# Kernel tuning notes

Hardware: AMD Instinct MI355X
Metric: run time of the kernel (lower is better)

Reference implementation:

```python
import jax, jax.numpy as jnp
import numpy as np
from jax import lax

N_Q = 4          # kernel_size**2 for Q_conv(kernel_size=2)
DIM = 16         # 2**N_Q statevector dimension
N_LAYERS = 3

# --- static circuit constants -------------------------------------------

def _cnot_np(c, t):
    # PennyLane convention: wire 0 is the most-significant bit.
    M = np.zeros((DIM, DIM), np.complex64)
    for s in range(DIM):
        s2 = s ^ (1 << (N_Q - 1 - t)) if (s >> (N_Q - 1 - c)) & 1 else s
        M[s2, s] = 1.0
    return jnp.asarray(M)

# StronglyEntanglingLayers: layer l uses range r = l % (n_wires-1) + 1
_CNOTS = {r: [_cnot_np(i, (i + r) % N_Q) for i in range(N_Q)] for r in (1, 2, 3)}

_ZDIAG = jnp.asarray(np.array(
    [[1.0 - 2.0 * ((s >> (N_Q - 1 - w)) & 1) for w in range(N_Q)] for s in range(DIM)],
    np.float32))  # (16, 4): diag of PauliZ on each wire


def _rot(p):
    # qml.Rot(phi, theta, omega) = RZ(omega) RY(theta) RZ(phi)
    phi, th, om = p[0], p[1], p[2]
    c, s = jnp.cos(th / 2), jnp.sin(th / 2)
    r0 = jnp.stack([jnp.exp(-1j * (phi + om) / 2) * c, -jnp.exp(1j * (phi - om) / 2) * s])
    r1 = jnp.stack([jnp.exp(-1j * (phi - om) / 2) * s, jnp.exp(1j * (phi + om) / 2) * c])
    return jnp.stack([r0, r1]).astype(jnp.complex64)


def _circuit_unitary(qw):
    # qw: (3, 4, 3). One StronglyEntanglingLayers block of 3 layers,
    # which the qnode applies n_layers=3 times with the SAME weights.
    U = jnp.eye(DIM, dtype=jnp.complex64)
    for l in range(N_LAYERS):
        L = _rot(qw[l, 0])
        for q in range(1, N_Q):
            L = jnp.kron(L, _rot(qw[l, q]))
        for C in _CNOTS[l + 1]:
            L = C @ L
        U = L @ U
    return U @ U @ U


def _quanv(x, qw):
    # x: (B, 1, 44, 44); k = stride = 2 -> non-overlapping 2x2 patches.
    B, H = x.shape[0], x.shape[-1]
    o = H // 2  # 22
    patches = x.reshape(B, o, 2, o, 2).transpose(0, 1, 3, 2, 4).reshape(-1, 4)
    # AngleEmbedding (RX) on |0000> gives a product state.
    a = jnp.cos(patches / 2).astype(jnp.complex64)
    b = (-1j * jnp.sin(patches / 2)).astype(jnp.complex64)
    w = jnp.stack([a, b], axis=-1)  # (N, 4, 2)
    psi0 = jnp.einsum('na,nb,nc,nd->nabcd', w[:, 0], w[:, 1], w[:, 2], w[:, 3]).reshape(-1, DIM)
    psi = psi0 @ _circuit_unitary(qw).T  # (N, 16)
    probs = psi.real ** 2 + psi.imag ** 2
    e = probs @ _ZDIAG  # (N, 4) expvals of PauliZ per wire
    return e.reshape(B, o * o, N_Q).transpose(0, 2, 1).reshape(B, N_Q, o, o).astype(x.dtype)


def _conv(x, w, b, stride):
    y = lax.conv_general_dilated(x, w, (stride, stride), 'VALID',
                                 dimension_numbers=('NCHW', 'OIHW', 'NCHW'))
    return y + b[None, :, None, None]


def _maxpool(x, k, s):
    return lax.reduce_window(x, -jnp.inf, lax.max, (1, 1, k, k), (1, 1, s, s), 'VALID')


def setup_inputs() -> dict:
    key = jax.random.key(0)
    ks = jax.random.split(key, 18)
    B = 256
    f32 = jnp.float32
    return {
        'x': jax.random.normal(ks[0], (B, 1, 186, 186), f32),
        'conv1_w': jax.random.normal(ks[1], (1, 1, 8, 8), f32) * 0.1,
        'conv1_b': jax.random.normal(ks[2], (1,), f32) * 0.05,
        'q_w': jax.random.uniform(ks[3], (3, 4, 3), f32, 0.0, 2.0 * np.pi),
        'conv2_w': jax.random.normal(ks[4], (32, 4, 4, 4), f32) * 0.1,
        'conv2_b': jax.random.normal(ks[5], (32,), f32) * 0.05,
        'conv3_w': jax.random.normal(ks[6], (64, 32, 4, 4), f32) * 0.05,
        'conv3_b': jax.random.normal(ks[7], (64,), f32) * 0.05,
        'conv4_w': jax.random.normal(ks[8], (128, 64, 4, 4), f32) * 0.03,
        'conv4_b': jax.random.normal(ks[9], (128,), f32) * 0.05,
        'fc1_w': jax.random.normal(ks[10], (128, 3200), f32) * 0.02,
        'fc1_b': jax.random.normal(ks[11], (128,), f32) * 0.05,
        'fc2_w': jax.random.normal(ks[12], (64, 128), f32) * 0.09,
        'fc2_b': jax.random.normal(ks[13], (64,), f32) * 0.05,
        'fc3_w': jax.random.normal(ks[14], (16, 64), f32) * 0.12,
        'fc3_b': jax.random.normal(ks[15], (16,), f32) * 0.05,
        'fc4_w': jax.random.normal(ks[16], (2, 16), f32) * 0.25,
        'fc4_b': jax.random.normal(ks[17], (2,), f32) * 0.05,
    }


def reference(x, conv1_w, conv1_b, q_w, conv2_w, conv2_b, conv3_w, conv3_b,
              conv4_w, conv4_b, fc1_w, fc1_b, fc2_w, fc2_b, fc3_w, fc3_b,
              fc4_w, fc4_b):
    h = _maxpool(jnp.tanh(_conv(x, conv1_w, conv1_b, 2)), 4, 2) * (np.pi / 2)
    h = jax.nn.relu(_quanv(h, q_w))                       # (B, 4, 22, 22)
    h = _maxpool(jax.nn.relu(_conv(h, conv2_w, conv2_b, 1)), 4, 1)
    h = _maxpool(jax.nn.relu(_conv(h, conv3_w, conv3_b, 1)), 2, 1)
    h = jax.nn.relu(_conv(h, conv4_w, conv4_b, 2))        # (B, 128, 5, 5)
    h = h.reshape(h.shape[0], -1)
    h = jax.nn.relu(h @ fc1_w.T + fc1_b)   # dropout: eval mode = identity
    h = jax.nn.relu(h @ fc2_w.T + fc2_b)
    h = jax.nn.relu(h @ fc3_w.T + fc3_b)
    return jax.nn.log_softmax(h @ fc4_w.T + fc4_b, axis=1)
```

## Files before the change

kernel.cpp:

```cpp
#include <hip/hip_runtime.h>
#include <hip/hip_bf16.h>
#include <math.h>


__device__ __forceinline__ float2 cmul(float2 a, float2 b) {
    return make_float2(a.x * b.x - a.y * b.y, a.x * b.y + a.y * b.x);
}
__device__ __forceinline__ float2 cfma(float2 a, float2 b, float2 acc) {
    acc.x += a.x * b.x - a.y * b.y;
    acc.y += a.x * b.y + a.y * b.x;
    return acc;
}

__global__ __launch_bounds__(256) void k_build_V(const float* __restrict__ qw,
                                                 float2* __restrict__ Vout) {
    __shared__ float2 rot[3][4][2][2];
    __shared__ float2 L[16][16];
    __shared__ float2 U[16][16];
    __shared__ float2 T[16][16];

    int tid = threadIdx.x;
    if (tid < 12) {
        int l = tid >> 2, q = tid & 3;
        float phi = qw[(l * 4 + q) * 3 + 0];
        float th  = qw[(l * 4 + q) * 3 + 1];
        float om  = qw[(l * 4 + q) * 3 + 2];
        float c, s;
        sincosf(0.5f * th, &s, &c);
        float sa, ca, sb, cb;
        sincosf(0.5f * (phi + om), &sa, &ca);
        sincosf(0.5f * (phi - om), &sb, &cb);
        rot[l][q][0][0] = make_float2( ca * c, -sa * c);
        rot[l][q][0][1] = make_float2(-cb * s, -sb * s);
        rot[l][q][1][0] = make_float2( cb * s, -sb * s);
        rot[l][q][1][1] = make_float2( ca * c,  sa * c);
    }
    int s = tid >> 4, t = tid & 15;
    U[s][t] = make_float2((s == t) ? 1.f : 0.f, 0.f);
    __syncthreads();

    for (int l = 0; l < 3; ++l) {
        int r = l + 1;
        int ss = s;
        for (int i = 3; i >= 0; --i) {
            int c_ = i, t_ = (i + r) & 3;
            if ((ss >> (3 - c_)) & 1) ss ^= 1 << (3 - t_);
        }
        float2 v = make_float2(1.f, 0.f);
        #pragma unroll
        for (int q = 0; q < 4; ++q) {
            int bs = (ss >> (3 - q)) & 1;
            int bt = (t  >> (3 - q)) & 1;
            v = cmul(v, rot[l][q][bs][bt]);
        }
        L[s][t] = v;
        __syncthreads();
        float2 acc = make_float2(0.f, 0.f);
        #pragma unroll
        for (int k = 0; k < 16; ++k) acc = cfma(L[s][k], U[k][t], acc);
        T[s][t] = acc;
        __syncthreads();
        U[s][t] = T[s][t];
        __syncthreads();
    }
    float2 acc = make_float2(0.f, 0.f);
    #pragma unroll
    for (int k = 0; k < 16; ++k) acc = cfma(U[s][k], U[k][t], acc);
    T[s][t] = acc;
    __syncthreads();
    acc = make_float2(0.f, 0.f);
    #pragma unroll
    for (int k = 0; k < 16; ++k) acc = cfma(T[s][k], U[k][t], acc);
    int pc = __popc(t) & 3;
    float2 v;
    if      (pc == 0) v = acc;
    else if (pc == 1) v = make_float2( acc.y, -acc.x);
    else if (pc == 2) v = make_float2(-acc.x, -acc.y);
    else              v = make_float2(-acc.y,  acc.x);
    Vout[s * 16 + t] = v;
}

__global__ __launch_bounds__(256) void k_wtrans(const float* __restrict__ w3,
                                                const float* __restrict__ w4,
                                                float* __restrict__ wt3,
                                                float* __restrict__ wt4) {
    int idx = blockIdx.x * 256 + threadIdx.x;
    if (idx < 32768) {
        int oc = idx & 63, tap = (idx >> 6) & 15, ic = idx >> 10;
        wt3[idx] = w3[oc * 512 + ic * 16 + tap];
    } else {
        int o = idx - 32768;
        int oc = o & 127, tap = (o >> 7) & 15, ic = o >> 11;
        wt4[o] = w4[oc * 1024 + ic * 16 + tap];
    }
}

__global__ __launch_bounds__(256) void k_conv1d(const float* __restrict__ x,
                                                const float* __restrict__ w,
                                                const float* __restrict__ bias,
                                                float* __restrict__ y) {
    int idx = blockIdx.x * 256 + threadIdx.x;
    int j = idx % 90;
    int t = idx / 90;
    int i = t % 90;
    int b = t / 90;
    const float* xb = x + b * 34596 + (2 * i) * 186 + 2 * j;
    float acc = bias[0];
    #pragma unroll
    for (int u = 0; u < 8; ++u) {
        const float* rp = xb + u * 186;
        float2 p0 = *(const float2*)(rp + 0);
        float2 p1 = *(const float2*)(rp + 2);
        float2 p2 = *(const float2*)(rp + 4);
        float2 p3 = *(const float2*)(rp + 6);
        acc = fmaf(w[u * 8 + 0], p0.x, acc);
        acc = fmaf(w[u * 8 + 1], p0.y, acc);
        acc = fmaf(w[u * 8 + 2], p1.x, acc);
        acc = fmaf(w[u * 8 + 3], p1.y, acc);
        acc = fmaf(w[u * 8 + 4], p2.x, acc);
        acc = fmaf(w[u * 8 + 5], p2.y, acc);
        acc = fmaf(w[u * 8 + 6], p3.x, acc);
        acc = fmaf(w[u * 8 + 7], p3.y, acc);
    }
    y[idx] = tanhf(acc);
}

__global__ __launch_bounds__(256) void k_pool1(const float* __restrict__ y,
                                               float* __restrict__ p) {
    int idx = blockIdx.x * 256 + threadIdx.x;
    int j = idx % 44;
    int t = idx / 44;
    int i = t % 44;
    int b = t / 44;
    const float* yb = y + b * 8100 + (2 * i) * 90 + 2 * j;
    float m = -INFINITY;
    #pragma unroll
    for (int u = 0; u < 4; ++u)
        #pragma unroll
        for (int v = 0; v < 4; ++v)
            m = fmaxf(m, yb[u * 90 + v]);
    p[idx] = m * 1.57079632679489662f;
}

__global__ __launch_bounds__(256) void k_quanv(const float* __restrict__ p,
                                               const float2* __restrict__ Vg,
                                               float* __restrict__ o) {
    __shared__ float2 V[256];
    V[threadIdx.x] = Vg[threadIdx.x];
    __syncthreads();

    int idx = blockIdx.x * 256 + threadIdx.x;
    int j = idx % 22;
    int t = idx / 22;
    int i = t % 22;
    int b = t / 22;
    const float* pb = p + b * 1936 + (2 * i) * 44 + 2 * j;
    float a0 = pb[0], a1 = pb[1], a2 = pb[44], a3 = pb[45];

    float cs[4], sn[4];
    sincosf(0.5f * a0, &sn[0], &cs[0]);
    sincosf(0.5f * a1, &sn[1], &cs[1]);
    sincosf(0.5f * a2, &sn[2], &cs[2]);
    sincosf(0.5f * a3, &sn[3], &cs[3]);

    float c[16];
    #pragma unroll
    for (int tt = 0; tt < 16; ++tt) {
        c[tt] = ((tt & 8) ? sn[0] : cs[0]) * ((tt & 4) ? sn[1] : cs[1]) *
                ((tt & 2) ? sn[2] : cs[2]) * ((tt & 1) ? sn[3] : cs[3]);
    }

    float e0 = 0.f, e1 = 0.f, e2 = 0.f, e3 = 0.f;
    #pragma unroll
    for (int s = 0; s < 16; ++s) {
        float re = 0.f, im = 0.f;
        #pragma unroll
        for (int tt = 0; tt < 16; ++tt) {
            float2 v = V[s * 16 + tt];
            re = fmaf(v.x, c[tt], re);
            im = fmaf(v.y, c[tt], im);
        }
        float pr = re * re + im * im;
        e0 += (s & 8) ? -pr : pr;
        e1 += (s & 4) ? -pr : pr;
        e2 += (s & 2) ? -pr : pr;
        e3 += (s & 1) ? -pr : pr;
    }
    float* ob = o + b * (4 * 484) + i * 22 + j;
    ob[0]    = fmaxf(e0, 0.f);
    ob[484]  = fmaxf(e1, 0.f);
    ob[968]  = fmaxf(e2, 0.f);
    ob[1452] = fmaxf(e3, 0.f);
}

__global__ __launch_bounds__(640) void k_conv2t(const float* __restrict__ x,
                                                const float* __restrict__ w,
                                                const float* __restrict__ bias,
                                                float* __restrict__ y) {
    __shared__ float Xs[4 * 22 * 28];
    __shared__ float Ws[32 * 68];
    int b = blockIdx.x;
    int tid = threadIdx.x;

    const float* xb = x + b * 1936;
    for (int k = tid; k < 1936; k += 640) {
        int ic = k / 484, rem = k % 484;
        int r = rem / 22, c = rem % 22;
        Xs[ic * 616 + r * 28 + c] = xb[k];
    }
    for (int k = tid; k < 2048; k += 640) {
        Ws[(k >> 6) * 68 + (k & 63)] = w[k];
    }
    __syncthreads();

    if (tid < 608) {
        int oc = tid / 19, i = tid % 19;
        float acc[19];
        float bv = bias[oc];
        #pragma unroll
        for (int j = 0; j < 19; ++j) acc[j] = bv;
        const float* wr = &Ws[oc * 68];
        #pragma unroll
        for (int ic = 0; ic < 4; ++ic) {
            #pragma unroll
            for (int u = 0; u < 4; ++u) {
                const float* rp = &Xs[ic * 616 + (i + u) * 28];
                float xr[22];
                #pragma unroll
                for (int k = 0; k < 5; ++k)
                    *(float4*)&xr[4 * k] = *(const float4*)(rp + 4 * k);
                *(float2*)&xr[20] = *(const float2*)(rp + 20);
                float4 wv = *(const float4*)(wr + ic * 16 + u * 4);
                #pragma unroll
                for (int j = 0; j < 19; ++j) {
                    acc[j] = fmaf(wv.x, xr[j],     acc[j]);
                    acc[j] = fmaf(wv.y, xr[j + 1], acc[j]);
                    acc[j] = fmaf(wv.z, xr[j + 2], acc[j]);
                    acc[j] = fmaf(wv.w, xr[j + 3], acc[j]);
                }
            }
        }
        float* yp = y + b * 11552 + oc * 361 + i * 19;
        #pragma unroll
        for (int j = 0; j < 19; ++j) yp[j] = fmaxf(acc[j], 0.f);
    }
}

__global__ __launch_bounds__(256) void k_pool2(const float* __restrict__ x,
                                               float* __restrict__ y) {
    int idx = blockIdx.x * 256 + threadIdx.x;
    int j = idx % 16;
    int t = idx / 16;
    int i = t % 16;
    int c = t / 16;
    const float* xb = x + c * 361 + i * 19 + j;
    float m = -INFINITY;
    #pragma unroll
    for (int u = 0; u < 4; ++u)
        #pragma unroll
        for (int v = 0; v < 4; ++v)
            m = fmaxf(m, xb[u * 19 + v]);
    y[idx] = m;
}

__global__ __launch_bounds__(448) void k_conv3x(const float* __restrict__ x,
                                                const float* __restrict__ wt3,
                                                const float* __restrict__ bias,
                                                float* __restrict__ y) {
    __shared__ float Xs[32 * 200];
    __shared__ float Rs[224 * 26];
    int bid = blockIdx.x;
    int b = bid >> 1, h = bid & 1;
    int r0 = h * 7;
    int nr = 7 - h;
    int tid = threadIdx.x;

    const float* xb = x + b * 8192 + r0 * 16;
    #pragma unroll
    for (int it = 0; it < 3; ++it) {
        int k = it * 448 + tid;
        if (k < 1280) {
            int ic = k / 40, rem = k % 40;
            int r = rem >> 2, c4 = rem & 3;
            if (r0 + r < 16) {
                float4 v = *(const float4*)(xb + ic * 256 + r * 16 + c4 * 4);
                *(float4*)(&Xs[ic * 200 + r * 20 + c4 * 4]) = v;
            }
        }
    }
    __syncthreads();

    int kg = (tid >= 224) ? 1 : 0;
    int t2 = tid - kg * 224;
    int ocp = t2 & 31, il = t2 >> 5;
    int oc0 = ocp * 2;

    float acc0[13], acc1[13];
    #pragma unroll
    for (int j = 0; j < 13; ++j) { acc0[j] = 0.f; acc1[j] = 0.f; }

    const float* wb = wt3 + kg * 16384 + oc0;
    for (int k = 0; k < 16; ++k) {
        const float* wp = wb + k * 1024;
        float2 cw[16];
        #pragma unroll
        for (int t = 0; t < 16; ++t) cw[t] = *(const float2*)(wp + t * 64);

        const float* xc = &Xs[(kg * 16 + k) * 200 + il * 20];
        #pragma unroll
        for (int u = 0; u < 4; ++u) {
            float xr[16];
            const float* rp = xc + u * 20;
            #pragma unroll
            for (int kk = 0; kk < 4; ++kk)
                *(float4*)&xr[4 * kk] = *(const float4*)(rp + 4 * kk);
            #pragma unroll
            for (int j = 0; j < 13; ++j) {
                #pragma unroll
                for (int v = 0; v < 4; ++v) {
                    acc0[j] = fmaf(cw[u * 4 + v].x, xr[j + v], acc0[j]);
                    acc1[j] = fmaf(cw[u * 4 + v].y, xr[j + v], acc1[j]);
                }
            }
        }
    }

    if (kg == 1) {
        float* rp = &Rs[t2 * 26];
        #pragma unroll
        for (int j = 0; j < 13; ++j) { rp[j] = acc0[j]; rp[13 + j] = acc1[j]; }
    }
    __syncthreads();

    if (kg == 0 && il < nr) {
        const float* rp = &Rs[t2 * 26];
        float bv0 = bias[oc0], bv1 = bias[oc0 + 1];
        float* yp = y + b * 10816 + oc0 * 169 + (r0 + il) * 13;
        #pragma unroll
        for (int j = 0; j < 13; ++j) {
            yp[j]       = fmaxf(acc0[j] + rp[j]      + bv0, 0.f);
            yp[169 + j] = fmaxf(acc1[j] + rp[13 + j] + bv1, 0.f);
        }
    }
}

__global__ __launch_bounds__(256) void k_pool3(const float* __restrict__ x,
                                               float* __restrict__ y) {
    int idx = blockIdx.x * 256 + threadIdx.x;
    int j = idx % 12;
    int t = idx / 12;
    int i = t % 12;
    int c = t / 12;
    const float* xb = x + c * 169 + i * 13 + j;
    float m = fmaxf(fmaxf(xb[0], xb[1]), fmaxf(xb[13], xb[14]));
    y[idx] = m;
}

__global__ __launch_bounds__(640) void k_conv4s(const float* __restrict__ x,
                                                const float* __restrict__ wt4,
                                                float* __restrict__ part) {
    __shared__ float Xs[32 * 144];
    __shared__ float Rs[320 * 10];
    int bid = blockIdx.x;
    int b = bid >> 1, kq = bid & 1;
    int tid = threadIdx.x;

    const float* xb = x + b * 9216 + kq * 4608;
    for (int k = tid; k < 1152; k += 640)
        *(float4*)&Xs[k * 4] = *(const float4*)(xb + k * 4);
    __syncthreads();

    int kg = (tid >= 320) ? 1 : 0;
    int t2 = tid - kg * 320;
    int ocp = t2 & 63, i = t2 >> 6;
    int oc0 = ocp * 2;

    float acc0[5], acc1[5];
    #pragma unroll
    for (int j = 0; j < 5; ++j) { acc0[j] = 0.f; acc1[j] = 0.f; }

    const float* wb = wt4 + kq * 65536 + kg * 32768 + oc0;
    for (int k = 0; k < 16; ++k) {
        const float* wp = wb + k * 2048;
        float2 cw[16];
        #pragma unroll
        for (int t = 0; t < 16; ++t) cw[t] = *(const float2*)(wp + t * 128);

        const float* xc = &Xs[(kg * 16 + k) * 144];
        #pragma unroll
        for (int u = 0; u < 4; ++u) {
            const float* rp = xc + (2 * i + u) * 12;
            float xr[12];
            #pragma unroll
            for (int kk = 0; kk < 3; ++kk)
                *(float4*)&xr[4 * kk] = *(const float4*)(rp + 4 * kk);
            #pragma unroll
            for (int j = 0; j < 5; ++j) {
                #pragma unroll
                for (int v = 0; v < 4; ++v) {
                    acc0[j] = fmaf(cw[u * 4 + v].x, xr[2 * j + v], acc0[j]);
                    acc1[j] = fmaf(cw[u * 4 + v].y, xr[2 * j + v], acc1[j]);
                }
            }
        }
    }

    if (kg == 1) {
        float* rp = &Rs[t2 * 10];
        #pragma unroll
        for (int j = 0; j < 5; ++j) { rp[j] = acc0[j]; rp[5 + j] = acc1[j]; }
    }
    __syncthreads();

    if (kg == 0) {
        const float* rp = &Rs[t2 * 10];
        float* pp = part + kq * 819200 + b * 3200 + oc0 * 25 + i * 5;
        #pragma unroll
        for (int j = 0; j < 5; ++j) {
            pp[j]      = acc0[j] + rp[j];
            pp[25 + j] = acc1[j] + rp[5 + j];
        }
    }
}

__global__ __launch_bounds__(256) void k_c4red(const float* __restrict__ part,
                                               const float* __restrict__ bias,
                                               float* __restrict__ y) {
    int idx = blockIdx.x * 256 + threadIdx.x;
    float s = part[idx] + part[idx + 819200];
    int oc = (idx / 25) & 127;
    y[idx] = fmaxf(s + bias[oc], 0.f);
}

__global__ __launch_bounds__(256) void k_fc1t(const float* __restrict__ x,
                                              const float* __restrict__ w,
                                              const float* __restrict__ bias,
                                              float* __restrict__ y) {
    __shared__ float Ls[4][32][65];
    int bid = blockIdx.x;
    int ig = bid >> 2, ocg = bid & 3;
    int imgB = ig * 4, ocB = ocg * 32;
    int tid = threadIdx.x, lane = tid & 63, wv = tid >> 6;
    int ocW = ocB + wv * 8;

    float acc[8][4];
    #pragma unroll
    for (int o = 0; o < 8; ++o)
        #pragma unroll
        for (int m = 0; m < 4; ++m) acc[o][m] = 0.f;

    for (int it = 0; it < 25; ++it) {
        int k = it * 128 + lane * 2;
        float2 xv[4];
        #pragma unroll
        for (int m = 0; m < 4; ++m)
            xv[m] = *(const float2*)&x[(imgB + m) * 3200 + k];
        #pragma unroll
        for (int o = 0; o < 8; ++o) {
            float2 wvv = *(const float2*)&w[(ocW + o) * 3200 + k];
            #pragma unroll
            for (int m = 0; m < 4; ++m) {
                acc[o][m] = fmaf(wvv.x, xv[m].x, acc[o][m]);
                acc[o][m] = fmaf(wvv.y, xv[m].y, acc[o][m]);
            }
        }
    }
    #pragma unroll
    for (int o = 0; o < 8; ++o)
        #pragma unroll
        for (int m = 0; m < 4; ++m)
            Ls[wv][o * 4 + m][lane] = acc[o][m];
    __syncthreads();

    if (tid < 128) {
        int w2 = tid >> 5, r = tid & 31;
        const float* p = Ls[w2][r];
        float s = 0.f;
        #pragma unroll
        for (int c = 0; c < 64; ++c) s += p[c];
        int o = r >> 2, m = r & 3;
        int oc = ocB + w2 * 8 + o;
        y[(imgB + m) * 128 + oc] = fmaxf(s + bias[oc], 0.f);
    }
}

__global__ __launch_bounds__(64) void k_fc_tail(const float* __restrict__ x,
                                                const float* __restrict__ w2,
                                                const float* __restrict__ b2,
                                                const float* __restrict__ w3,
                                                const float* __restrict__ b3,
                                                const float* __restrict__ w4,
                                                const float* __restrict__ b4,
                                                float* __restrict__ out) {
    __shared__ float xs[128], h2[64], h3[16];
    int img = blockIdx.x;
    int lane = threadIdx.x;

    *(float2*)&xs[lane * 2] = *(const float2*)&x[img * 128 + lane * 2];
    __syncthreads();

    float a = b2[lane];
    const float4* wp = (const float4*)&w2[lane * 128];
    const float4* xp = (const float4*)xs;
    #pragma unroll
    for (int k = 0; k < 32; ++k) {
        float4 wv = wp[k], xv = xp[k];
        a = fmaf(wv.x, xv.x, a);
        a = fmaf(wv.y, xv.y, a);
        a = fmaf(wv.z, xv.z, a);
        a = fmaf(wv.w, xv.w, a);
    }
    h2[lane] = fmaxf(a, 0.f);
    __syncthreads();

    if (lane < 16) {
        float a3 = b3[lane];
        const float4* w3p = (const float4*)&w3[lane * 64];
        const float4* h2p = (const float4*)h2;
        #pragma unroll
        for (int k = 0; k < 16; ++k) {
            float4 wv = w3p[k], xv = h2p[k];
            a3 = fmaf(wv.x, xv.x, a3);
            a3 = fmaf(wv.y, xv.y, a3);
            a3 = fmaf(wv.z, xv.z, a3);
            a3 = fmaf(wv.w, xv.w, a3);
        }
        h3[lane] = fmaxf(a3, 0.f);
    }
    __syncthreads();

    if (lane == 0) {
        float z0 = b4[0], z1 = b4[1];
        #pragma unroll
        for (int k = 0; k < 16; ++k) {
            z0 = fmaf(w4[k],      h3[k], z0);
            z1 = fmaf(w4[16 + k], h3[k], z1);
        }
        float m = fmaxf(z0, z1);
        float lse = m + logf(expf(z0 - m) + expf(z1 - m));
        out[img * 2 + 0] = z0 - lse;
        out[img * 2 + 1] = z1 - lse;
    }
}

extern "C" void kernel_launch(void* const* d_in, const int* in_sizes, int n_in,
                              void* d_out, int out_size, void* d_ws, size_t ws_size,
                              hipStream_t stream) {
    const float* x       = (const float*)d_in[0];
    const float* conv1_w = (const float*)d_in[1];
    const float* conv1_b = (const float*)d_in[2];
    const float* q_w     = (const float*)d_in[3];
    const float* conv2_w = (const float*)d_in[4];
    const float* conv2_b = (const float*)d_in[5];
    const float* conv3_w = (const float*)d_in[6];
    const float* conv3_b = (const float*)d_in[7];
    const float* conv4_w = (const float*)d_in[8];
    const float* conv4_b = (const float*)d_in[9];
    const float* fc1_w   = (const float*)d_in[10];
    const float* fc1_b   = (const float*)d_in[11];
    const float* fc2_w   = (const float*)d_in[12];
    const float* fc2_b   = (const float*)d_in[13];
    const float* fc3_w   = (const float*)d_in[14];
    const float* fc3_b   = (const float*)d_in[15];
    const float* fc4_w   = (const float*)d_in[16];
    const float* fc4_b   = (const float*)d_in[17];
    float* out = (float*)d_out;

    char* ws = (char*)d_ws;
    float2* V  = (float2*)ws;
    float* A   = (float*)(ws + 4096);
    float* B   = (float*)(ws + 9441280);
    float* WT3 = (float*)(ws + 21950464);
    float* WT4 = (float*)(ws + 22089728);

    k_build_V<<<1, 256, 0, stream>>>(q_w, V);
    k_wtrans<<<640, 256, 0, stream>>>(conv3_w, conv4_w, WT3, WT4);
    k_conv1d<<<8100, 256, 0, stream>>>(x, conv1_w, conv1_b, A);
    k_pool1<<<1936, 256, 0, stream>>>(A, B);
    k_quanv<<<484, 256, 0, stream>>>(B, V, A);
    k_conv2t<<<256, 640, 0, stream>>>(A, conv2_w, conv2_b, B);
    k_pool2<<<8192, 256, 0, stream>>>(B, A);
    k_conv3x<<<512, 448, 0, stream>>>(A, WT3, conv3_b, B);
    k_pool3<<<9216, 256, 0, stream>>>(B, A);
    k_conv4s<<<512, 640, 0, stream>>>(A, WT4, B);
    k_c4red<<<3200, 256, 0, stream>>>(B, conv4_b, A);
    k_fc1t<<<256, 256, 0, stream>>>(A, fc1_w, fc1_b, B);
    k_fc_tail<<<256, 64, 0, stream>>>(B, fc2_w, fc2_b, fc3_w, fc3_b,
                                      fc4_w, fc4_b, out);
}
```

Measured before the change: 185.6 us.

## Fuse maxpools into quanv and conv4 loaders; prefetch conv weights in registers

```diff
diff --git a/kernel.cpp b/kernel.cpp
--- a/kernel.cpp
+++ b/kernel.cpp
@@ -125,26 +125,9 @@
     y[idx] = tanhf(acc);
 }
 
-__global__ __launch_bounds__(256) void k_pool1(const float* __restrict__ y,
-                                               float* __restrict__ p) {
-    int idx = blockIdx.x * 256 + threadIdx.x;
-    int j = idx % 44;
-    int t = idx / 44;
-    int i = t % 44;
-    int b = t / 44;
-    const float* yb = y + b * 8100 + (2 * i) * 90 + 2 * j;
-    float m = -INFINITY;
-    #pragma unroll
-    for (int u = 0; u < 4; ++u)
-        #pragma unroll
-        for (int v = 0; v < 4; ++v)
-            m = fmaxf(m, yb[u * 90 + v]);
-    p[idx] = m * 1.57079632679489662f;
-}
-
-__global__ __launch_bounds__(256) void k_quanv(const float* __restrict__ p,
-                                               const float2* __restrict__ Vg,
-                                               float* __restrict__ o) {
+__global__ __launch_bounds__(256) void k_quanvp(const float* __restrict__ y,
+                                                const float2* __restrict__ Vg,
+                                                float* __restrict__ o) {
     __shared__ float2 V[256];
     V[threadIdx.x] = Vg[threadIdx.x];
     __syncthreads();
@@ -154,8 +137,26 @@
     int t = idx / 22;
     int i = t % 22;
     int b = t / 22;
-    const float* pb = p + b * 1936 + (2 * i) * 44 + 2 * j;
-    float a0 = pb[0], a1 = pb[1], a2 = pb[44], a3 = pb[45];
+
+    const float* yb = y + b * 8100 + (4 * i) * 90 + 4 * j;
+    float ra[6], rb[6];
+    #pragma unroll
+    for (int r = 0; r < 6; ++r) {
+        const float* rp = yb + r * 90;
+        float2 p0 = *(const float2*)(rp);
+        float2 p1 = *(const float2*)(rp + 2);
+        float2 p2 = *(const float2*)(rp + 4);
+        float m01 = fmaxf(p0.x, p0.y);
+        float m23 = fmaxf(p1.x, p1.y);
+        float m45 = fmaxf(p2.x, p2.y);
+        ra[r] = fmaxf(m01, m23);
+        rb[r] = fmaxf(m23, m45);
+    }
+    const float S = 1.57079632679489662f;
+    float a0 = S * fmaxf(fmaxf(ra[0], ra[1]), fmaxf(ra[2], ra[3]));
+    float a1 = S * fmaxf(fmaxf(rb[0], rb[1]), fmaxf(rb[2], rb[3]));
+    float a2 = S * fmaxf(fmaxf(ra[2], ra[3]), fmaxf(ra[4], ra[5]));
+    float a3 = S * fmaxf(fmaxf(rb[2], rb[3]), fmaxf(rb[4], rb[5]));
 
     float cs[4], sn[4];
     sincosf(0.5f * a0, &sn[0], &cs[0]);
@@ -300,11 +301,16 @@
     for (int j = 0; j < 13; ++j) { acc0[j] = 0.f; acc1[j] = 0.f; }
 
     const float* wb = wt3 + kg * 16384 + oc0;
+    float2 cw[16];
+    #pragma unroll
+    for (int t = 0; t < 16; ++t) cw[t] = *(const float2*)(wb + t * 64);
+
     for (int k = 0; k < 16; ++k) {
-        const float* wp = wb + k * 1024;
-        float2 cw[16];
-        #pragma unroll
-        for (int t = 0; t < 16; ++t) cw[t] = *(const float2*)(wp + t * 64);
+        int kn = (k < 15) ? k + 1 : 15;
+        const float* wn = wb + kn * 1024;
+        float2 nw[16];
+        #pragma unroll
+        for (int t = 0; t < 16; ++t) nw[t] = *(const float2*)(wn + t * 64);
 
         const float* xc = &Xs[(kg * 16 + k) * 200 + il * 20];
         #pragma unroll
@@ -323,6 +329,8 @@
                 }
             }
         }
+        #pragma unroll
+        for (int t = 0; t < 16; ++t) cw[t] = nw[t];
     }
 
     if (kg == 1) {
@@ -344,19 +352,7 @@
     }
 }
 
-__global__ __launch_bounds__(256) void k_pool3(const float* __restrict__ x,
-                                               float* __restrict__ y) {
-    int idx = blockIdx.x * 256 + threadIdx.x;
-    int j = idx % 12;
-    int t = idx / 12;
-    int i = t % 12;
-    int c = t / 12;
-    const float* xb = x + c * 169 + i * 13 + j;
-    float m = fmaxf(fmaxf(xb[0], xb[1]), fmaxf(xb[13], xb[14]));
-    y[idx] = m;
-}
-
-__global__ __launch_bounds__(640) void k_conv4s(const float* __restrict__ x,
+__global__ __launch_bounds__(640) void k_conv4s(const float* __restrict__ x3,
                                                 const float* __restrict__ wt4,
                                                 float* __restrict__ part) {
     __shared__ float Xs[32 * 144];
@@ -365,9 +361,14 @@
     int b = bid >> 1, kq = bid & 1;
     int tid = threadIdx.x;
 
-    const float* xb = x + b * 9216 + kq * 4608;
-    for (int k = tid; k < 1152; k += 640)
-        *(float4*)&Xs[k * 4] = *(const float4*)(xb + k * 4);
+    const float* gb = x3 + b * 10816 + kq * 32 * 169;
+    for (int k = tid; k < 4608; k += 640) {
+        int ic = k / 144, rc = k % 144;
+        int r = rc / 12, c = rc % 12;
+        const float* g = gb + ic * 169 + r * 13 + c;
+        float m = fmaxf(fmaxf(g[0], g[1]), fmaxf(g[13], g[14]));
+        Xs[k] = m;
+    }
     __syncthreads();
 
     int kg = (tid >= 320) ? 1 : 0;
@@ -380,11 +381,16 @@
     for (int j = 0; j < 5; ++j) { acc0[j] = 0.f; acc1[j] = 0.f; }
 
     const float* wb = wt4 + kq * 65536 + kg * 32768 + oc0;
+    float2 cw[16];
+    #pragma unroll
+    for (int t = 0; t < 16; ++t) cw[t] = *(const float2*)(wb + t * 128);
+
     for (int k = 0; k < 16; ++k) {
-        const float* wp = wb + k * 2048;
-        float2 cw[16];
-        #pragma unroll
-        for (int t = 0; t < 16; ++t) cw[t] = *(const float2*)(wp + t * 128);
+        int kn = (k < 15) ? k + 1 : 15;
+        const float* wn = wb + kn * 2048;
+        float2 nw[16];
+        #pragma unroll
+        for (int t = 0; t < 16; ++t) nw[t] = *(const float2*)(wn + t * 128);
 
         const float* xc = &Xs[(kg * 16 + k) * 144];
         #pragma unroll
@@ -403,6 +409,8 @@
                 }
             }
         }
+        #pragma unroll
+        for (int t = 0; t < 16; ++t) cw[t] = nw[t];
     }
 
     if (kg == 1) {
@@ -569,19 +577,17 @@
     char* ws = (char*)d_ws;
     float2* V  = (float2*)ws;
     float* A   = (float*)(ws + 4096);
-    float* B   = (float*)(ws + 9441280);
-    float* WT3 = (float*)(ws + 21950464);
-    float* WT4 = (float*)(ws + 22089728);
+    float* B   = (float*)(ws + 12587008);
+    float* WT3 = (float*)(ws + 21499904);
+    float* WT4 = (float*)(ws + 21639168);
 
     k_build_V<<<1, 256, 0, stream>>>(q_w, V);
     k_wtrans<<<640, 256, 0, stream>>>(conv3_w, conv4_w, WT3, WT4);
     k_conv1d<<<8100, 256, 0, stream>>>(x, conv1_w, conv1_b, A);
-    k_pool1<<<1936, 256, 0, stream>>>(A, B);
-    k_quanv<<<484, 256, 0, stream>>>(B, V, A);
-    k_conv2t<<<256, 640, 0, stream>>>(A, conv2_w, conv2_b, B);
-    k_pool2<<<8192, 256, 0, stream>>>(B, A);
-    k_conv3x<<<512, 448, 0, stream>>>(A, WT3, conv3_b, B);
-    k_pool3<<<9216, 256, 0, stream>>>(B, A);
+    k_quanvp<<<484, 256, 0, stream>>>(A, V, B);
+    k_conv2t<<<256, 640, 0, stream>>>(B, conv2_w, conv2_b, A);
+    k_pool2<<<8192, 256, 0, stream>>>(A, B);
+    k_conv3x<<<512, 448, 0, stream>>>(B, WT3, conv3_b, A);
     k_conv4s<<<512, 640, 0, stream>>>(A, WT4, B);
     k_c4red<<<3200, 256, 0, stream>>>(B, conv4_b, A);
     k_fc1t<<<256, 256, 0, stream>>>(A, fc1_w, fc1_b, B);
```

Result: no change. 186.5 us (+0.5%).
